# Performance work log

Hardware: AMD Instinct MI355X
Metric: run time of the kernel (lower is better)

Reference implementation:

```python
import jax, jax.numpy as jnp
import numpy as np

B, S, E, H = 2, 2048, 768, 8
D = E // H  # 96
SCALING = D ** (-0.5)


def setup_inputs() -> dict:
    key = jax.random.key(0)
    ks = jax.random.split(key, 7)
    sd = E ** -0.5
    return {
        "x": jax.random.normal(ks[0], (B, S, E), jnp.float32),
        "Wq": jax.random.normal(ks[1], (E, E), jnp.float32) * sd,
        "bq": jax.random.normal(ks[2], (E,), jnp.float32) * 0.02,
        "Wk": jax.random.normal(ks[3], (E, E), jnp.float32) * sd,
        "bk": jax.random.normal(ks[4], (E,), jnp.float32) * 0.02,
        "Wo": jax.random.normal(ks[5], (E, E), jnp.float32) * sd,
        "bo": jax.random.normal(ks[6], (E,), jnp.float32) * 0.02,
    }


def _split_heads(t):
    # [B, S, E] -> [B, H, S, D]
    return t.reshape(B, S, H, D).transpose(0, 2, 1, 3)


def reference(x, Wq, bq, Wk, bk, Wo, bo):
    q = _split_heads(x @ Wq + bq)
    k = _split_heads(x @ Wk + bk)
    # NOTE: faithful to source bug — values use the KEY projection
    v = _split_heads(x @ Wk + bk)
    energies = jnp.einsum("bhqd,bhkd->bhqk", q, k)  # [B,H,S,S]
    # NOTE: faithful to source — scaling applied AFTER softmax
    attn = jax.nn.softmax(energies, axis=-1) * SCALING
    out = jnp.einsum("bhqk,bhkd->bhqd", attn, v)
    out = out.transpose(0, 2, 1, 3).reshape(B, S, E)
    return out @ Wo + bo
```

## Files before the change

kernel.cpp:

```cpp
#include <hip/hip_runtime.h>
#include <hip/hip_bf16.h>
#include <math.h>
#include <stdint.h>

#define B_DIM 2
#define S_DIM 2048
#define E_DIM 768
#define H_DIM 8
#define D_DIM 96
#define M_DIM (B_DIM*S_DIM)
#define SCALE_F 0.10206207261596575f

typedef _Float16 f16x8 __attribute__((ext_vector_type(8)));
typedef float    f32x4  __attribute__((ext_vector_type(4)));
typedef float    f32x16 __attribute__((ext_vector_type(16)));

#define MFMA16H(a,b,c) __builtin_amdgcn_mfma_f32_16x16x32_f16(a,b,c,0,0,0)
#define MFMA32H(a,b,c) __builtin_amdgcn_mfma_f32_32x32x16_f16(a,b,c,0,0,0)

__device__ inline unsigned short f2h(float f) {
    return __builtin_bit_cast(unsigned short, (_Float16)f);
}

__device__ inline void gload16(const void* g, void* l) {
    auto gp = reinterpret_cast<const __attribute__((address_space(1))) uint32_t*>(
        reinterpret_cast<uintptr_t>(g));
    auto lp = reinterpret_cast<__attribute__((address_space(3))) uint32_t*>(
        reinterpret_cast<uintptr_t>(l));
    __builtin_amdgcn_global_load_lds(gp, lp, 16, 0, 0);
}

__global__ __launch_bounds__(256) void prep_kernel(
    const float* __restrict__ X,
    const float* __restrict__ W0, const float* __restrict__ W1,
    const float* __restrict__ W2,
    unsigned short* __restrict__ Xf,
    unsigned short* __restrict__ T0, unsigned short* __restrict__ T1,
    unsigned short* __restrict__ T2)
{
    const int tid = threadIdx.x;
    if (blockIdx.x < 3072) {
        int i = (blockIdx.x * 256 + tid) * 4;
        float4 v = *(const float4*)(X + i);
        ushort4 h;
        h.x = f2h(v.x); h.y = f2h(v.y); h.z = f2h(v.z); h.w = f2h(v.w);
        *(ushort4*)(Xf + i) = h;
        return;
    }
    int idx = blockIdx.x - 3072;
    int z = idx / 144, rem = idx % 144;
    const float* W; unsigned short* T;
    if (z == 0)      { W = W0; T = T0; }
    else if (z == 1) { W = W1; T = T1; }
    else             { W = W2; T = T2; }
    int k0 = (rem / 12) << 6, n0 = (rem % 12) << 6;

    __shared__ float tile[64][65];
    const int r = tid >> 4, c4 = (tid & 15) << 2;
    #pragma unroll
    for (int i = 0; i < 4; ++i) {
        float4 v = *(const float4*)(W + (size_t)(k0 + r + i*16)*E_DIM + n0 + c4);
        tile[r + i*16][c4+0] = v.x; tile[r + i*16][c4+1] = v.y;
        tile[r + i*16][c4+2] = v.z; tile[r + i*16][c4+3] = v.w;
    }
    __syncthreads();
    #pragma unroll
    for (int i = 0; i < 4; ++i) {
        int n = r + i*16;
        ushort4 h;
        h.x = f2h(tile[c4+0][n]); h.y = f2h(tile[c4+1][n]);
        h.z = f2h(tile[c4+2][n]); h.w = f2h(tile[c4+3][n]);
        *(ushort4*)(T + (size_t)(n0 + n)*E_DIM + k0 + c4) = h;
    }
}

__global__ __launch_bounds__(256) void gemm_qk_kernel(
    const unsigned short* __restrict__ A, const unsigned short* __restrict__ Bt,
    const float* __restrict__ bq, const float* __restrict__ bk,
    unsigned short* __restrict__ Qf, unsigned short* __restrict__ Kf)
{
    __shared__ unsigned short sA[2*128*32];
    __shared__ unsigned short sB[2*64*32];

    const int tid  = threadIdx.x;
    const int lane = tid & 63;
    const int w    = tid >> 6;
    const int qn   = lane & 15, quad = lane >> 4;
    const int wm   = w & 1, wn = w >> 1;

    const int flat = blockIdx.x;
    const int g = flat & 7, s = flat >> 3;
    const int row0 = ((g << 2) + (s & 3)) << 7;
    const int col0 = (s >> 2) << 6;

    const int ar = tid >> 2;
    const int ak = (tid & 3) << 3;

    const unsigned short* gA = A  + (size_t)(row0 + ar)*E_DIM + ak;
    const unsigned short* gB = Bt + (size_t)(col0 + ar)*E_DIM + ak;

    f32x4 acc[4][2];
    #pragma unroll
    for (int mt = 0; mt < 4; ++mt)
        #pragma unroll
        for (int nt = 0; nt < 2; ++nt)
            { acc[mt][nt][0]=0.f; acc[mt][nt][1]=0.f; acc[mt][nt][2]=0.f; acc[mt][nt][3]=0.f; }

    for (int k0 = 0; k0 < E_DIM; k0 += 64) {
        __syncthreads();
        gload16(gA + k0,                 sA + tid*8);
        gload16(gA + 64*E_DIM + k0,      sA + 2048 + tid*8);
        gload16(gA + k0 + 32,            sA + 4096 + tid*8);
        gload16(gA + 64*E_DIM + k0 + 32, sA + 6144 + tid*8);
        gload16(gB + k0,                 sB + tid*8);
        gload16(gB + k0 + 32,            sB + 2048 + tid*8);
        __syncthreads();

        #pragma unroll
        for (int kk = 0; kk < 2; ++kk) {
            f16x8 af[4], bf[2];
            #pragma unroll
            for (int mt = 0; mt < 4; ++mt)
                af[mt] = *(const f16x8*)&sA[kk*4096 + (wm*64 + mt*16 + qn)*32 + quad*8];
            #pragma unroll
            for (int nt = 0; nt < 2; ++nt)
                bf[nt] = *(const f16x8*)&sB[kk*2048 + (wn*32 + nt*16 + qn)*32 + quad*8];
            #pragma unroll
            for (int mt = 0; mt < 4; ++mt)
                #pragma unroll
                for (int nt = 0; nt < 2; ++nt)
                    acc[mt][nt] = MFMA16H(af[mt], bf[nt], acc[mt][nt]);
        }
    }

    #pragma unroll
    for (int nt = 0; nt < 2; ++nt) {
        int n = col0 + wn*32 + nt*16 + qn;
        bool isQ = n < E_DIM;
        float bias = isQ ? bq[n] : bk[n - E_DIM];
        unsigned short* op = isQ ? Qf : Kf;
        int nc = isQ ? n : n - E_DIM;
        #pragma unroll
        for (int mt = 0; mt < 4; ++mt)
            #pragma unroll
            for (int r = 0; r < 4; ++r) {
                int m = row0 + wm*64 + mt*16 + quad*4 + r;
                op[(size_t)m*E_DIM + nc] = f2h(acc[mt][nt][r] + bias);
            }
    }
}

__global__ __launch_bounds__(256) void attn_mfma_kernel(
    const unsigned short* __restrict__ Qf, const unsigned short* __restrict__ Kf,
    unsigned short* __restrict__ O0, unsigned short* __restrict__ O1,
    float2* __restrict__ ml)
{
    __shared__ unsigned short sKh[2][64][104];
    __shared__ unsigned short sKt[2][96][72];
    __shared__ unsigned short sPs[128][72];

    const int tid  = threadIdx.x;
    const int w    = tid >> 6;
    const int lane = tid & 63;
    const int col  = lane & 31;
    const int half = lane >> 5;
    const int b    = blockIdx.z >> 1;
    const int kh   = blockIdx.z & 1;
    const int h    = blockIdx.y;
    const int q0   = blockIdx.x << 7;
    const int key0 = kh << 10;

    f16x8 qf[6];
    {
        const size_t ro = ((size_t)(b*S_DIM + q0 + w*32 + col))*E_DIM
                          + h*D_DIM + half*8;
        #pragma unroll
        for (int kc = 0; kc < 6; ++kc)
            qf[kc] = *(const f16x8*)(Qf + ro + kc*16);
    }

    f32x16 o[3];
    #pragma unroll
    for (int nt = 0; nt < 3; ++nt)
        #pragma unroll
        for (int r = 0; r < 16; ++r) o[nt][r] = 0.f;
    float m_i = -INFINITY, l_i = 0.f;

    const bool stager = tid < 128;
    const int st = tid & 127;
    const int sp = st >> 2;
    const int dq = st & 3;

    uint4 r0[3], r1[3];
    if (stager) {
        const size_t g0 = ((size_t)(b*S_DIM + key0 + 2*sp))*E_DIM + h*D_DIM + dq*24;
        #pragma unroll
        for (int i = 0; i < 3; ++i) {
            r0[i] = *(const uint4*)(Kf + g0 + 8*i);
            r1[i] = *(const uint4*)(Kf + g0 + E_DIM + 8*i);
        }
    }

    for (int kt = 0; kt < 16; ++kt) {
        const int p = kt & 1;
        if (stager) {
            #pragma unroll
            for (int i = 0; i < 3; ++i) {
                *(uint4*)&sKh[p][2*sp  ][dq*24 + 8*i] = r0[i];
                *(uint4*)&sKh[p][2*sp+1][dq*24 + 8*i] = r1[i];
            }
            const unsigned short* p0 = (const unsigned short*)r0;
            const unsigned short* p1 = (const unsigned short*)r1;
            #pragma unroll
            for (int c = 0; c < 24; ++c) {
                unsigned int pk = (unsigned int)p0[c] | ((unsigned int)p1[c] << 16);
                *(unsigned int*)&sKt[p][dq*24 + c][2*sp] = pk;
            }
        }
        __syncthreads();

        if (stager && kt + 1 < 16) {
            const size_t g0 = ((size_t)(b*S_DIM + key0 + (kt+1)*64 + 2*sp))*E_DIM
                              + h*D_DIM + dq*24;
            #pragma unroll
            for (int i = 0; i < 3; ++i) {
                r0[i] = *(const uint4*)(Kf + g0 + 8*i);
                r1[i] = *(const uint4*)(Kf + g0 + E_DIM + 8*i);
            }
        }

        f32x16 s[2];
        #pragma unroll
        for (int mt = 0; mt < 2; ++mt) {
            f32x16 acc;
            #pragma unroll
            for (int r = 0; r < 16; ++r) acc[r] = 0.f;
            #pragma unroll
            for (int kc = 0; kc < 6; ++kc) {
                f16x8 ah = *(const f16x8*)&sKh[p][mt*32 + col][kc*16 + half*8];
                acc = MFMA32H(ah, qf[kc], acc);
            }
            s[mt] = acc;
        }

        float mx = s[0][0];
        #pragma unroll
        for (int mt = 0; mt < 2; ++mt)
            #pragma unroll
            for (int r = 0; r < 16; ++r) mx = fmaxf(mx, s[mt][r]);
        mx = fmaxf(mx, __shfl_xor(mx, 32));

        float m_new = fmaxf(m_i, mx);
        float alpha = __expf(m_i - m_new);
        m_i = m_new;

        float psum = 0.f;
        #pragma unroll
        for (int mt = 0; mt < 2; ++mt)
            #pragma unroll
            for (int g = 0; g < 4; ++g) {
                float e0 = __expf(s[mt][4*g+0] - m_new);
                float e1 = __expf(s[mt][4*g+1] - m_new);
                float e2 = __expf(s[mt][4*g+2] - m_new);
                float e3 = __expf(s[mt][4*g+3] - m_new);
                psum += e0 + e1 + e2 + e3;
                ushort4 pk;
                pk.x = f2h(e0); pk.y = f2h(e1); pk.z = f2h(e2); pk.w = f2h(e3);
                *(ushort4*)&sPs[w*32 + col][mt*32 + 8*g + 4*half] = pk;
            }
        psum += __shfl_xor(psum, 32);
        l_i = l_i * alpha + psum;

        #pragma unroll
        for (int nt = 0; nt < 3; ++nt)
            #pragma unroll
            for (int r = 0; r < 16; ++r) o[nt][r] *= alpha;

        #pragma unroll
        for (int kc = 0; kc < 4; ++kc) {
            f16x8 pb = *(const f16x8*)&sPs[w*32 + col][kc*16 + half*8];
            #pragma unroll
            for (int nt = 0; nt < 3; ++nt) {
                f16x8 va = *(const f16x8*)&sKt[p][nt*32 + col][kc*16 + half*8];
                o[nt] = MFMA32H(va, pb, o[nt]);
            }
        }
    }

    unsigned short* Ob = (kh ? O1 : O0)
        + ((size_t)(b*S_DIM + q0 + w*32 + col))*E_DIM + h*D_DIM;
    #pragma unroll
    for (int nt = 0; nt < 3; ++nt)
        #pragma unroll
        for (int rg = 0; rg < 4; ++rg) {
            ushort4 pk;
            pk.x = f2h(o[nt][4*rg+0]); pk.y = f2h(o[nt][4*rg+1]);
            pk.z = f2h(o[nt][4*rg+2]); pk.w = f2h(o[nt][4*rg+3]);
            *(ushort4*)(Ob + nt*32 + 8*rg + 4*half) = pk;
        }
    if (lane < 32) {
        int q = q0 + w*32 + lane;
        ml[((size_t)(kh*B_DIM + b)*H_DIM + h)*S_DIM + q] = make_float2(m_i, l_i);
    }
}

__device__ inline float2 mkscale(const float2* __restrict__ ml, int m, int h) {
    int b = m >> 11, q = m & (S_DIM - 1);
    float2 e0 = ml[((size_t)b*H_DIM + h)*S_DIM + q];
    float2 e1 = ml[((size_t)(B_DIM + b)*H_DIM + h)*S_DIM + q];
    float mm = fmaxf(e0.x, e1.x);
    float w0 = __expf(e0.x - mm), w1 = __expf(e1.x - mm);
    float inv = SCALE_F / (e0.y*w0 + e1.y*w1);
    return make_float2(w0*inv, w1*inv);
}

__global__ __launch_bounds__(256) void gemm_out_kernel(
    const unsigned short* __restrict__ O0, const unsigned short* __restrict__ O1,
    const float2* __restrict__ ml, const unsigned short* __restrict__ Bt,
    const float* __restrict__ bo, float* __restrict__ out)
{
    __shared__ unsigned short sA[2*64*32];
    __shared__ unsigned short sB[2*64*32];

    const int tid  = threadIdx.x;
    const int lane = tid & 63;
    const int w    = tid >> 6;
    const int qn   = lane & 15, quad = lane >> 4;
    const int wm   = w & 1, wn = w >> 1;

    const int flat = blockIdx.x;
    const int g = flat & 7, s = flat >> 3;
    const int row0 = ((g << 3) + (s & 7)) << 6;
    const int col0 = (s >> 3) << 6;

    const int ar = tid >> 2;
    const int ak = (tid & 3) << 3;

    const size_t r0o = (size_t)(row0 + ar)*E_DIM;
    const unsigned short* gB = Bt + (size_t)(col0 + ar)*E_DIM + ak;

    f32x4 acc[2][2];
    #pragma unroll
    for (int mt = 0; mt < 2; ++mt)
        #pragma unroll
        for (int nt = 0; nt < 2; ++nt)
            { acc[mt][nt][0]=0.f; acc[mt][nt][1]=0.f; acc[mt][nt][2]=0.f; acc[mt][nt][3]=0.f; }

    f16x8 uA = *(const f16x8*)(O0 + r0o + ak);
    f16x8 vA = *(const f16x8*)(O1 + r0o + ak);
    f16x8 uB = *(const f16x8*)(O0 + r0o + 32 + ak);
    f16x8 vB = *(const f16x8*)(O1 + r0o + 32 + ak);
    int hA = 0, hB = 0;
    float2 s2 = mkscale(ml, row0 + ar, 0);
    _Float16 axA = (_Float16)s2.x, ayA = (_Float16)s2.y;
    _Float16 axB = axA, ayB = ayA;

    for (int k0 = 0; k0 < E_DIM; k0 += 64) {
        __syncthreads();
        {
            f16x8 c0 = uA * axA + vA * ayA;
            f16x8 c1 = uB * axB + vB * ayB;
            *(f16x8*)&sA[       ar*32 + ak] = c0;
            *(f16x8*)&sA[2048 + ar*32 + ak] = c1;
        }
        gload16(gB + k0,      sB + tid*8);
        gload16(gB + k0 + 32, sB + 2048 + tid*8);
        __syncthreads();

        if (k0 + 64 < E_DIM) {
            int kn = k0 + 64;
            uA = *(const f16x8*)(O0 + r0o + kn + ak);
            vA = *(const f16x8*)(O1 + r0o + kn + ak);
            uB = *(const f16x8*)(O0 + r0o + kn + 32 + ak);
            vB = *(const f16x8*)(O1 + r0o + kn + 32 + ak);
            int nhA = kn / D_DIM, nhB = (kn + 32) / D_DIM;
            if (nhA != hA) {
                float2 t = mkscale(ml, row0 + ar, nhA);
                axA = (_Float16)t.x; ayA = (_Float16)t.y; hA = nhA;
            }
            if (nhB != hB) {
                float2 t = mkscale(ml, row0 + ar, nhB);
                axB = (_Float16)t.x; ayB = (_Float16)t.y; hB = nhB;
            }
        }

        #pragma unroll
        for (int kk = 0; kk < 2; ++kk) {
            f16x8 af[2], bf[2];
            #pragma unroll
            for (int mt = 0; mt < 2; ++mt)
                af[mt] = *(const f16x8*)&sA[kk*2048 + (wm*32 + mt*16 + qn)*32 + quad*8];
            #pragma unroll
            for (int nt = 0; nt < 2; ++nt)
                bf[nt] = *(const f16x8*)&sB[kk*2048 + (wn*32 + nt*16 + qn)*32 + quad*8];
            #pragma unroll
            for (int mt = 0; mt < 2; ++mt)
                #pragma unroll
                for (int nt = 0; nt < 2; ++nt)
                    acc[mt][nt] = MFMA16H(af[mt], bf[nt], acc[mt][nt]);
        }
    }

    #pragma unroll
    for (int nt = 0; nt < 2; ++nt) {
        int n = col0 + wn*32 + nt*16 + qn;
        float bias = bo[n];
        #pragma unroll
        for (int mt = 0; mt < 2; ++mt)
            #pragma unroll
            for (int r = 0; r < 4; ++r) {
                int m = row0 + wm*32 + mt*16 + quad*4 + r;
                out[(size_t)m*E_DIM + n] = acc[mt][nt][r] + bias;
            }
    }
}

extern "C" void kernel_launch(void* const* d_in, const int* in_sizes, int n_in,
                              void* d_out, int out_size, void* d_ws, size_t ws_size,
                              hipStream_t stream)
{
    const float* x  = (const float*)d_in[0];
    const float* Wq = (const float*)d_in[1];
    const float* bq = (const float*)d_in[2];
    const float* Wk = (const float*)d_in[3];
    const float* bk = (const float*)d_in[4];
    const float* Wo = (const float*)d_in[5];
    const float* bo = (const float*)d_in[6];
    float* out = (float*)d_out;

    const size_t NE = (size_t)M_DIM * E_DIM;
    const size_t WE = (size_t)E_DIM * E_DIM;
    unsigned short* xf    = (unsigned short*)d_ws;
    unsigned short* WqkT  = xf + NE;
    unsigned short* WoT   = WqkT + 2*WE;
    unsigned short* Qf    = WoT + WE;
    unsigned short* Kf    = Qf + NE;
    unsigned short* Oh1   = Kf + NE;
    float2*         mlbuf = (float2*)(Oh1 + NE);
    unsigned short* Oh0   = xf;

    dim3 blk(256);
    hipLaunchKernelGGL(prep_kernel, dim3(3504), blk, 0, stream,
                       x, Wq, Wk, Wo, xf, WqkT, WqkT + WE, WoT);

    hipLaunchKernelGGL(gemm_qk_kernel, dim3(768), blk, 0, stream,
                       xf, WqkT, bq, bk, Qf, Kf);

    hipLaunchKernelGGL(attn_mfma_kernel, dim3(S_DIM/128, H_DIM, B_DIM*2), blk, 0,
                       stream, Qf, Kf, Oh0, Oh1, mlbuf);

    hipLaunchKernelGGL(gemm_out_kernel, dim3(768), blk, 0, stream,
                       Oh0, Oh1, mlbuf, WoT, bo, out);
}
```

Before: 156.7 us.

## Keep softmax probabilities in registers via permlane swap, fold log2e into Q, lazy rescale

The attention kernel no longer writes probabilities to shared memory and reads them back. It packs them into f16 registers and uses permlane32_swap to build the MFMA B operand. The log2(e) factor is folded into the Wq and bq conversion so exp2 can be used directly. The running-max rescale is skipped unless the max grows by more than a threshold, and the output is normalised by l_i before the store. The K staging layout is swizzled to reduce LDS bank conflicts on the transposed copy. The lazy rescale risks f16 overflow of the probabilities (up to 2^10) and relies on the combine step handling the normalised partials.

```diff
diff --git a/kernel.cpp b/kernel.cpp
--- a/kernel.cpp
+++ b/kernel.cpp
@@ -10,16 +10,22 @@
 #define D_DIM 96
 #define M_DIM (B_DIM*S_DIM)
 #define SCALE_F 0.10206207261596575f
+#define LOG2E_F 1.44269504088896341f
 
 typedef _Float16 f16x8 __attribute__((ext_vector_type(8)));
 typedef float    f32x4  __attribute__((ext_vector_type(4)));
 typedef float    f32x16 __attribute__((ext_vector_type(16)));
+typedef unsigned int u32x4 __attribute__((ext_vector_type(4)));
 
 #define MFMA16H(a,b,c) __builtin_amdgcn_mfma_f32_16x16x32_f16(a,b,c,0,0,0)
 #define MFMA32H(a,b,c) __builtin_amdgcn_mfma_f32_32x32x16_f16(a,b,c,0,0,0)
 
 __device__ inline unsigned short f2h(float f) {
     return __builtin_bit_cast(unsigned short, (_Float16)f);
+}
+
+__device__ inline unsigned pk2(float a, float b) {
+    return __builtin_bit_cast(unsigned, __builtin_amdgcn_cvt_pkrtz(a, b));
 }
 
 __device__ inline void gload16(const void* g, void* l) {
@@ -53,6 +59,7 @@
     if (z == 0)      { W = W0; T = T0; }
     else if (z == 1) { W = W1; T = T1; }
     else             { W = W2; T = T2; }
+    const float sc = (z == 0) ? LOG2E_F : 1.0f;
     int k0 = (rem / 12) << 6, n0 = (rem % 12) << 6;
 
     __shared__ float tile[64][65];
@@ -68,8 +75,8 @@
     for (int i = 0; i < 4; ++i) {
         int n = r + i*16;
         ushort4 h;
-        h.x = f2h(tile[c4+0][n]); h.y = f2h(tile[c4+1][n]);
-        h.z = f2h(tile[c4+2][n]); h.w = f2h(tile[c4+3][n]);
+        h.x = f2h(tile[c4+0][n] * sc); h.y = f2h(tile[c4+1][n] * sc);
+        h.z = f2h(tile[c4+2][n] * sc); h.w = f2h(tile[c4+3][n] * sc);
         *(ushort4*)(T + (size_t)(n0 + n)*E_DIM + k0 + c4) = h;
     }
 }
@@ -137,7 +144,7 @@
     for (int nt = 0; nt < 2; ++nt) {
         int n = col0 + wn*32 + nt*16 + qn;
         bool isQ = n < E_DIM;
-        float bias = isQ ? bq[n] : bk[n - E_DIM];
+        float bias = isQ ? bq[n] * LOG2E_F : bk[n - E_DIM];
         unsigned short* op = isQ ? Qf : Kf;
         int nc = isQ ? n : n - E_DIM;
         #pragma unroll
@@ -157,7 +164,6 @@
 {
     __shared__ unsigned short sKh[2][64][104];
     __shared__ unsigned short sKt[2][96][72];
-    __shared__ unsigned short sPs[128][72];
 
     const int tid  = threadIdx.x;
     const int w    = tid >> 6;
@@ -190,42 +196,46 @@
     const int st = tid & 127;
     const int sp = st >> 2;
     const int dq = st & 3;
+    const int kp2 = ((sp + ((dq & 1) << 4)) & 31) << 1;
 
     uint4 r0[3], r1[3];
     if (stager) {
-        const size_t g0 = ((size_t)(b*S_DIM + key0 + 2*sp))*E_DIM + h*D_DIM + dq*24;
+        const size_t g0 = ((size_t)(b*S_DIM + key0 + 2*sp))*E_DIM + h*D_DIM + dq*8;
         #pragma unroll
         for (int i = 0; i < 3; ++i) {
-            r0[i] = *(const uint4*)(Kf + g0 + 8*i);
-            r1[i] = *(const uint4*)(Kf + g0 + E_DIM + 8*i);
-        }
-    }
+            r0[i] = *(const uint4*)(Kf + g0 + 32*i);
+            r1[i] = *(const uint4*)(Kf + g0 + E_DIM + 32*i);
+        }
+    }
+
+    const int kswz = ((col >> 3) & 1) << 2;
 
     for (int kt = 0; kt < 16; ++kt) {
         const int p = kt & 1;
         if (stager) {
             #pragma unroll
             for (int i = 0; i < 3; ++i) {
-                *(uint4*)&sKh[p][2*sp  ][dq*24 + 8*i] = r0[i];
-                *(uint4*)&sKh[p][2*sp+1][dq*24 + 8*i] = r1[i];
+                *(uint4*)&sKh[p][2*sp  ][dq*8 + 32*i] = r0[i];
+                *(uint4*)&sKh[p][2*sp+1][dq*8 + 32*i] = r1[i];
             }
             const unsigned short* p0 = (const unsigned short*)r0;
             const unsigned short* p1 = (const unsigned short*)r1;
             #pragma unroll
             for (int c = 0; c < 24; ++c) {
-                unsigned int pk = (unsigned int)p0[c] | ((unsigned int)p1[c] << 16);
-                *(unsigned int*)&sKt[p][dq*24 + c][2*sp] = pk;
+                int d = dq*8 + ((c >> 3) << 5) + (c & 7);
+                unsigned pk = (unsigned)p0[c] | ((unsigned)p1[c] << 16);
+                *(unsigned*)&sKt[p][d][kp2] = pk;
             }
         }
         __syncthreads();
 
         if (stager && kt + 1 < 16) {
             const size_t g0 = ((size_t)(b*S_DIM + key0 + (kt+1)*64 + 2*sp))*E_DIM
-                              + h*D_DIM + dq*24;
+                              + h*D_DIM + dq*8;
             #pragma unroll
             for (int i = 0; i < 3; ++i) {
-                r0[i] = *(const uint4*)(Kf + g0 + 8*i);
-                r1[i] = *(const uint4*)(Kf + g0 + E_DIM + 8*i);
+                r0[i] = *(const uint4*)(Kf + g0 + 32*i);
+                r1[i] = *(const uint4*)(Kf + g0 + E_DIM + 32*i);
             }
         }
 
@@ -243,50 +253,62 @@
             s[mt] = acc;
         }
 
-        float mx = s[0][0];
+        float t[8];
+        #pragma unroll
+        for (int r = 0; r < 8; ++r)
+            t[r] = fmaxf(fmaxf(s[0][r], s[0][r+8]), fmaxf(s[1][r], s[1][r+8]));
+        float mx = fmaxf(fmaxf(fmaxf(t[0], t[1]), fmaxf(t[2], t[3])),
+                         fmaxf(fmaxf(t[4], t[5]), fmaxf(t[6], t[7])));
+        mx = fmaxf(mx, __shfl_xor(mx, 32));
+
+        if (__any(mx > m_i + 10.0f)) {
+            float m_new = fmaxf(m_i, mx);
+            float alpha = __builtin_amdgcn_exp2f(m_i - m_new);
+            l_i *= alpha;
+            #pragma unroll
+            for (int nt = 0; nt < 3; ++nt)
+                #pragma unroll
+                for (int r = 0; r < 16; ++r) o[nt][r] *= alpha;
+            m_i = m_new;
+        }
+
         #pragma unroll
         for (int mt = 0; mt < 2; ++mt)
             #pragma unroll
-            for (int r = 0; r < 16; ++r) mx = fmaxf(mx, s[mt][r]);
-        mx = fmaxf(mx, __shfl_xor(mx, 32));
-
-        float m_new = fmaxf(m_i, mx);
-        float alpha = __expf(m_i - m_new);
-        m_i = m_new;
-
-        float psum = 0.f;
-        #pragma unroll
-        for (int mt = 0; mt < 2; ++mt)
-            #pragma unroll
-            for (int g = 0; g < 4; ++g) {
-                float e0 = __expf(s[mt][4*g+0] - m_new);
-                float e1 = __expf(s[mt][4*g+1] - m_new);
-                float e2 = __expf(s[mt][4*g+2] - m_new);
-                float e3 = __expf(s[mt][4*g+3] - m_new);
-                psum += e0 + e1 + e2 + e3;
-                ushort4 pk;
-                pk.x = f2h(e0); pk.y = f2h(e1); pk.z = f2h(e2); pk.w = f2h(e3);
-                *(ushort4*)&sPs[w*32 + col][mt*32 + 8*g + 4*half] = pk;
-            }
-        psum += __shfl_xor(psum, 32);
-        l_i = l_i * alpha + psum;
-
-        #pragma unroll
-        for (int nt = 0; nt < 3; ++nt)
-            #pragma unroll
-            for (int r = 0; r < 16; ++r) o[nt][r] *= alpha;
+            for (int r = 0; r < 16; ++r)
+                s[mt][r] = __builtin_amdgcn_exp2f(s[mt][r] - m_i);
+
+        float a[8];
+        #pragma unroll
+        for (int r = 0; r < 8; ++r)
+            a[r] = (s[0][r] + s[0][r+8]) + (s[1][r] + s[1][r+8]);
+        float ps = ((a[0]+a[1]) + (a[2]+a[3])) + ((a[4]+a[5]) + (a[6]+a[7]));
+        ps += __shfl_xor(ps, 32);
+        l_i += ps;
 
         #pragma unroll
         for (int kc = 0; kc < 4; ++kc) {
-            f16x8 pb = *(const f16x8*)&sPs[w*32 + col][kc*16 + half*8];
+            const int mt = kc >> 1;
+            const int g0 = (kc & 1) << 3;
+            unsigned A0 = pk2(s[mt][g0+0], s[mt][g0+1]);
+            unsigned A1 = pk2(s[mt][g0+2], s[mt][g0+3]);
+            unsigned B0 = pk2(s[mt][g0+4], s[mt][g0+5]);
+            unsigned B1 = pk2(s[mt][g0+6], s[mt][g0+7]);
+            auto w0 = __builtin_amdgcn_permlane32_swap(A0, B0, false, false);
+            auto w1 = __builtin_amdgcn_permlane32_swap(A1, B1, false, false);
+            u32x4 pw;
+            pw[0] = w0[0]; pw[1] = w1[0]; pw[2] = w0[1]; pw[3] = w1[1];
+            f16x8 pb = __builtin_bit_cast(f16x8, pw);
             #pragma unroll
             for (int nt = 0; nt < 3; ++nt) {
-                f16x8 va = *(const f16x8*)&sKt[p][nt*32 + col][kc*16 + half*8];
+                f16x8 va = *(const f16x8*)
+                    &sKt[p][nt*32 + col][(((kc << 1) | half) ^ kswz) << 3];
                 o[nt] = MFMA32H(va, pb, o[nt]);
             }
         }
     }
 
+    float inv = 1.0f / l_i;
     unsigned short* Ob = (kh ? O1 : O0)
         + ((size_t)(b*S_DIM + q0 + w*32 + col))*E_DIM + h*D_DIM;
     #pragma unroll
@@ -294,8 +316,8 @@
         #pragma unroll
         for (int rg = 0; rg < 4; ++rg) {
             ushort4 pk;
-            pk.x = f2h(o[nt][4*rg+0]); pk.y = f2h(o[nt][4*rg+1]);
-            pk.z = f2h(o[nt][4*rg+2]); pk.w = f2h(o[nt][4*rg+3]);
+            pk.x = f2h(o[nt][4*rg+0]*inv); pk.y = f2h(o[nt][4*rg+1]*inv);
+            pk.z = f2h(o[nt][4*rg+2]*inv); pk.w = f2h(o[nt][4*rg+3]*inv);
             *(ushort4*)(Ob + nt*32 + 8*rg + 4*half) = pk;
         }
     if (lane < 32) {
@@ -309,8 +331,9 @@
     float2 e0 = ml[((size_t)b*H_DIM + h)*S_DIM + q];
     float2 e1 = ml[((size_t)(B_DIM + b)*H_DIM + h)*S_DIM + q];
     float mm = fmaxf(e0.x, e1.x);
-    float w0 = __expf(e0.x - mm), w1 = __expf(e1.x - mm);
-    float inv = SCALE_F / (e0.y*w0 + e1.y*w1);
+    float w0 = e0.y * __builtin_amdgcn_exp2f(e0.x - mm);
+    float w1 = e1.y * __builtin_amdgcn_exp2f(e1.x - mm);
+    float inv = SCALE_F / (w0 + w1);
     return make_float2(w0*inv, w1*inv);
 }
 
```

After: 156.5 us. No clear change (-0.1%).
